# Performance work log

Measured on AMD Instinct MI355X. Metric: run time of the kernel, lower is better.

The kernel has to match this reference:

```python
import jax, jax.numpy as jnp
from jax import lax
import numpy as np

B, T, N, HORIZON = 64, 12, 512, 12
IN_DIM = 1; OUT_DIM = 1; YCOV = 1
RNN = 64; MEM_NUM = 20; MEM_DIM = 64; EMB = 10; CHEB_K = 3
DEC_DIM = RNN + MEM_DIM  # 128


def _xavier(key, shape):
    fan_in, fan_out = shape[0], shape[-1]
    std = float(np.sqrt(2.0 / (fan_in + fan_out)))
    return jax.random.normal(key, shape, dtype=jnp.float32) * std


def _cheb_feats(A, x, batched):
    mm = (lambda a, v: jnp.einsum('bnm,bmc->bnc', a, v)) if batched else (lambda a, v: jnp.einsum('nm,bmc->bnc', a, v))
    gs = [x, mm(A, x)]
    for _ in range(CHEB_K - 2):
        gs.append(2.0 * mm(A, gs[-1]) - gs[-2])
    return jnp.concatenate(gs, axis=-1)


def _agcn(x, A, W, b, batched):
    return _cheb_feats(A, x, batched) @ W + b


def _cell(x, state, A, Wg, bg, Wu, bu, batched):
    # AGCRN GRU cell
    hid = state.shape[-1]
    inp = jnp.concatenate([x, state], axis=-1)
    z_r = jax.nn.sigmoid(_agcn(inp, A, Wg, bg, batched))
    z, r = z_r[..., :hid], z_r[..., hid:]
    cand = jnp.concatenate([x, z * state], axis=-1)
    hc = jnp.tanh(_agcn(cand, A, Wu, bu, batched))
    return r * state + (1.0 - r) * hc


def _encode(x, A, Wg, bg, Wu, bu):
    # x: [B,T,N,C] -> last hidden state [B,N,RNN]
    xt = jnp.swapaxes(x, 0, 1)  # [T,B,N,C]
    init = jnp.zeros((x.shape[0], x.shape[2], RNN), x.dtype)
    def step(state, xt_):
        h = _cell(xt_, state, A, Wg, bg, Wu, bu, batched=False)
        return h, None
    h_t, _ = lax.scan(step, init, xt)
    return h_t


def _query_memory(h_t, Memory, Wq):
    q = h_t @ Wq                                   # [B,N,mem_dim]
    att = jax.nn.softmax(q @ Memory.T, axis=-1)    # [B,N,mem_num]
    value = att @ Memory                           # [B,N,mem_dim]
    _, ind = lax.top_k(att, 2)
    pos = Memory[ind[..., 0]]                      # [B,N,mem_dim]
    return value, pos


def setup_inputs() -> dict:
    key = jax.random.key(0)
    ks = jax.random.split(key, 20)
    x = jax.random.normal(ks[0], (B, T, N, IN_DIM), dtype=jnp.float32)
    x_cov = jax.random.normal(ks[1], (B, T, N, 1), dtype=jnp.float32)
    x_his = jax.random.normal(ks[2], (B, T, N, IN_DIM), dtype=jnp.float32)
    y_cov = jax.random.normal(ks[3], (B, HORIZON, N, YCOV), dtype=jnp.float32)
    a = jax.random.uniform(ks[4], (N, N), dtype=jnp.float32)
    adj = a / jnp.sum(a, axis=-1, keepdims=True)
    enc_in = IN_DIM + RNN
    dec_in = OUT_DIM + YCOV + DEC_DIM
    return {
        'x': x, 'x_cov': x_cov, 'x_his': x_his, 'y_cov': y_cov, 'adj': adj,
        'enc_gate_W': _xavier(ks[5], (CHEB_K * enc_in, 2 * RNN)),
        'enc_gate_b': jnp.zeros((2 * RNN,), jnp.float32),
        'enc_upd_W': _xavier(ks[6], (CHEB_K * enc_in, RNN)),
        'enc_upd_b': jnp.zeros((RNN,), jnp.float32),
        'dec_gate_W': _xavier(ks[7], (CHEB_K * dec_in, 2 * DEC_DIM)),
        'dec_gate_b': jnp.zeros((2 * DEC_DIM,), jnp.float32),
        'dec_upd_W': _xavier(ks[8], (CHEB_K * dec_in, DEC_DIM)),
        'dec_upd_b': jnp.zeros((DEC_DIM,), jnp.float32),
        'Memory': _xavier(ks[9], (MEM_NUM, MEM_DIM)),
        'Wq': _xavier(ks[10], (RNN, MEM_DIM)),
        'hyper_W': _xavier(ks[11], (DEC_DIM, EMB)),
        'hyper_b': jnp.zeros((EMB,), jnp.float32),
        'lat_W': _xavier(ks[12], (MEM_DIM, 1)),
        'lat_b': jnp.zeros((1,), jnp.float32),
        'proj_W': _xavier(ks[13], (DEC_DIM, OUT_DIM)),
        'proj_b': jnp.zeros((OUT_DIM,), jnp.float32),
    }


def reference(x, x_cov, x_his, y_cov, adj,
              enc_gate_W, enc_gate_b, enc_upd_W, enc_upd_b,
              dec_gate_W, dec_gate_b, dec_upd_W, dec_upd_b,
              Memory, Wq, hyper_W, hyper_b, lat_W, lat_b, proj_W, proj_b):
    # --- encoder on x and x_his (shared weights, single static support) ---
    h_t = _encode(x, adj, enc_gate_W, enc_gate_b, enc_upd_W, enc_upd_b)
    h_att, pos = _query_memory(h_t, Memory, Wq)
    h_his_t = _encode(x_his, adj, enc_gate_W, enc_gate_b, enc_upd_W, enc_upd_b)
    _, pos_his = _query_memory(h_his_t, Memory, Wq)
    # schema==1 latent distance head (sigmoid activation)
    latent_dis = jax.nn.sigmoid(((pos - pos_his) @ lat_W + lat_b)[..., 0])  # [B,N]
    # --- adaptive decoder support from hypernetwork ---
    h_aug = jnp.concatenate([h_t, h_att], axis=-1)          # [B,N,DEC_DIM]
    node_emb = h_aug @ hyper_W + hyper_b                    # [B,N,EMB]
    support = jax.nn.softmax(jax.nn.relu(jnp.einsum('bnc,bmc->bnm', node_emb, node_emb)), axis=-1)  # [B,N,N]
    # --- decoder rollout (inference path, no teacher forcing) ---
    go0 = jnp.zeros((x.shape[0], N, OUT_DIM), x.dtype)
    ycov_t = jnp.swapaxes(y_cov, 0, 1)  # [HORIZON,B,N,YCOV]
    def dec_step(carry, yc):
        go, h = carry
        xt = jnp.concatenate([go, yc], axis=-1)
        h = _cell(xt, h, support, dec_gate_W, dec_gate_b, dec_upd_W, dec_upd_b, batched=True)
        go = h @ proj_W + proj_b
        return (go, h), go
    _, outs = lax.scan(dec_step, (go0, h_aug), ycov_t)
    output = jnp.swapaxes(outs, 0, 1)  # [B,HORIZON,N,OUT_DIM]
    return output, latent_dis
```

## Files before the change

### kernel.cpp

```cpp
#include <hip/hip_runtime.h>
#include <hip/hip_bf16.h>


typedef __attribute__((ext_vector_type(8))) short s8v;
typedef __attribute__((ext_vector_type(4))) float f4v;
typedef __attribute__((ext_vector_type(4))) unsigned short u4v;

__device__ __forceinline__ float b2f(unsigned short u){
  union{unsigned int i; float f;} v; v.i = ((unsigned int)u)<<16; return v.f;
}
__device__ __forceinline__ unsigned short f2b(float f){
  union{float f; unsigned int i;} v; v.f = f;
  unsigned int r = v.i + 0x7fff + ((v.i >> 16) & 1);
  return (unsigned short)(r >> 16);
}

__global__ void k_zero16(uint4* p, int n){
  int i = blockIdx.x*256 + threadIdx.x;
  if (i < n) p[i] = make_uint4(0,0,0,0);
}


__global__ void k_reorderF(const float* __restrict__ W, float* __restrict__ Wr,
                           int HC, int NEX, int SEGW, int J){
  int idx = blockIdx.x*256 + threadIdx.x;
  int K = 3*SEGW;
  if (idx >= K*J) return;
  int k = idx / J, j = idx - k*J;
  int seg = k / SEGW, c = k - seg*SEGW;
  int CIN = HC + NEX;
  float v = 0.f;
  if (c < HC)       v = W[(size_t)(seg*CIN + NEX + c)*J + j];
  else if (c < CIN) v = W[(size_t)(seg*CIN + (c-HC))*J + j];
  Wr[(size_t)k*J + j] = v;
}

__global__ __launch_bounds__(256) void k_a2e(const float* __restrict__ A,
                                             float* __restrict__ A2e){
  __shared__ __align__(16) float As[32][132];
  __shared__ __align__(16) float Bs[32][132];
  int t = threadIdx.x;
  int r0 = (blockIdx.x & 3) * 128;
  int c0 = (blockIdx.x >> 2) * 128;
  int tr = t & 15, tc = t >> 4;
  float acc[8][8];
  #pragma unroll
  for (int i=0;i<8;i++)
    #pragma unroll
    for (int j=0;j<8;j++) acc[i][j]=0.f;
  for (int k0=0;k0<512;k0+=32){
    #pragma unroll
    for (int i=0;i<4;i++){
      int s = t + i*256;
      int r = s >> 3, kq = s & 7;
      float4 v = *(const float4*)(A + (size_t)(r0+r)*512 + k0 + kq*4);
      As[kq*4+0][r]=v.x; As[kq*4+1][r]=v.y; As[kq*4+2][r]=v.z; As[kq*4+3][r]=v.w;
    }
    #pragma unroll
    for (int i=0;i<4;i++){
      int s = t + i*256;
      int k = s >> 5, cq = s & 31;
      float4 v = *(const float4*)(A + (size_t)(k0+k)*512 + c0 + cq*4);
      *(float4*)&Bs[k][cq*4] = v;
    }
    __syncthreads();
    #pragma unroll 8
    for (int k=0;k<32;k++){
      float a[8], b[8];
      *(float4*)&a[0] = *(const float4*)&As[k][tr*4];
      *(float4*)&a[4] = *(const float4*)&As[k][64+tr*4];
      *(float4*)&b[0] = *(const float4*)&Bs[k][tc*4];
      *(float4*)&b[4] = *(const float4*)&Bs[k][64+tc*4];
      #pragma unroll
      for (int i=0;i<8;i++)
        #pragma unroll
        for (int j=0;j<8;j++) acc[i][j] += a[i]*b[j];
    }
    __syncthreads();
  }
  #pragma unroll
  for (int i=0;i<8;i++){
    int r = r0 + (i<4 ? tr*4+i : 64+tr*4+i-4);
    #pragma unroll
    for (int j=0;j<8;j++){
      int c = c0 + (j<4 ? tc*4+j : 64+tc*4+j-4);
      A2e[(size_t)r*512 + c] = 2.f*acc[i][j] - (r==c ? 1.f : 0.f);
    }
  }
}

__global__ __launch_bounds__(256,2) void k_mm2F(
    const float* __restrict__ A, const float* __restrict__ A2e,
    const float* __restrict__ hsrc,
    const float* __restrict__ xa, const float* __restrict__ xb,
    int tstep, float* __restrict__ feats)
{
  __shared__ __align__(16) float As[32][132];
  __shared__ __align__(16) float A2s[32][132];
  __shared__ __align__(16) float Bs[32][68];
  const int t = threadIdx.x;
  const int bb = blockIdx.z;
  const int n0 = blockIdx.x * 128;
  const int tr = t & 15, tc = t >> 4;
  const int xrow = t & 127, xmat = t >> 7;
  const float* xp = (bb < 64) ? (xa + ((size_t)bb*12 + tstep)*512)
                              : (xb + ((size_t)(bb-64)*12 + tstep)*512);
  float acc[2][2][4][4];
  #pragma unroll
  for (int m=0;m<2;m++)
    #pragma unroll
    for (int rg=0;rg<2;rg++)
      #pragma unroll
      for (int i=0;i<4;i++)
        #pragma unroll
        for (int j=0;j<4;j++) acc[m][rg][i][j]=0.f;
  float xacc = 0.f;

  for (int k0=0;k0<512;k0+=32){
    #pragma unroll
    for (int i=0;i<4;i++){
      int s = t + i*256;
      int r = s >> 3, kq = s & 7;
      float4 v = *(const float4*)(A + (size_t)(n0+r)*512 + k0 + kq*4);
      As[kq*4+0][r]=v.x; As[kq*4+1][r]=v.y; As[kq*4+2][r]=v.z; As[kq*4+3][r]=v.w;
      float4 w = *(const float4*)(A2e + (size_t)(n0+r)*512 + k0 + kq*4);
      A2s[kq*4+0][r]=w.x; A2s[kq*4+1][r]=w.y; A2s[kq*4+2][r]=w.z; A2s[kq*4+3][r]=w.w;
    }
    #pragma unroll
    for (int i=0;i<2;i++){
      int s = t + i*256;
      int k = s >> 4, cq = s & 15;
      float4 v = *(const float4*)(hsrc + (size_t)(bb*512 + k0 + k)*64 + cq*4);
      *(float4*)&Bs[k][cq*4] = v;
    }
    if (t < 32) Bs[t][64] = xp[k0 + t];
    __syncthreads();
    #pragma unroll 4
    for (int k=0;k<32;k++){
      float a1[8], a2[8], b[4];
      *(float4*)&a1[0] = *(const float4*)&As[k][tr*4];
      *(float4*)&a1[4] = *(const float4*)&As[k][64+tr*4];
      *(float4*)&a2[0] = *(const float4*)&A2s[k][tr*4];
      *(float4*)&a2[4] = *(const float4*)&A2s[k][64+tr*4];
      *(float4*)&b[0]  = *(const float4*)&Bs[k][tc*4];
      #pragma unroll
      for (int rg=0;rg<2;rg++)
        #pragma unroll
        for (int i=0;i<4;i++)
          #pragma unroll
          for (int j=0;j<4;j++){
            acc[0][rg][i][j] += a1[rg*4+i]*b[j];
            acc[1][rg][i][j] += a2[rg*4+i]*b[j];
          }
      xacc += (xmat ? A2s[k][xrow] : As[k][xrow]) * Bs[k][64];
    }
    if ((k0 >> 7) == (int)blockIdx.x){
      for (int s=t; s<544; s+=256){
        int k = s/17, q = s - k*17;
        float4 v;
        if (q < 16) v = *(const float4*)&Bs[k][q*4];
        else        v = make_float4(Bs[k][64], 0.f, 0.f, 0.f);
        *(float4*)(feats + (size_t)(bb*512 + k0 + k)*204 + q*4) = v;
      }
    }
    __syncthreads();
  }
  #pragma unroll
  for (int rg=0;rg<2;rg++){
    #pragma unroll
    for (int i=0;i<4;i++){
      int row = n0 + rg*64 + tr*4 + i;
      float* fr = feats + (size_t)(bb*512 + row)*204;
      float4 v;
      v.x=acc[0][rg][i][0]; v.y=acc[0][rg][i][1];
      v.z=acc[0][rg][i][2]; v.w=acc[0][rg][i][3];
      *(float4*)(fr + 68 + tc*4) = v;
      v.x=acc[1][rg][i][0]; v.y=acc[1][rg][i][1];
      v.z=acc[1][rg][i][2]; v.w=acc[1][rg][i][3];
      *(float4*)(fr + 136 + tc*4) = v;
    }
  }
  feats[(size_t)(bb*512 + n0 + xrow)*204 + (xmat ? 136 : 68) + 64] = xacc;
}

__global__ __launch_bounds__(256) void k_gwG(
    const float* __restrict__ feats, const float* __restrict__ Wr,
    const float* __restrict__ bias,
    const float* __restrict__ hbuf, float* __restrict__ zh, float* __restrict__ rbuf)
{
  __shared__ __align__(16) float As[17][132];
  __shared__ __align__(16) float Ws[17][132];
  const int t = threadIdx.x;
  const int row0 = blockIdx.x * 128;
  const int tr = t & 15, tc = t >> 4;
  float acc[2][2][4][4];
  #pragma unroll
  for (int rg=0;rg<2;rg++)
    #pragma unroll
    for (int cg=0;cg<2;cg++)
      #pragma unroll
      for (int i=0;i<4;i++)
        #pragma unroll
        for (int j=0;j<4;j++) acc[rg][cg][i][j]=0.f;
  for (int kc=0; kc<204; kc+=17){
    for (int s=t; s<2176; s+=256){
      int r = s/17, k = s - r*17;
      As[k][r] = feats[(size_t)(row0+r)*204 + kc + k];
    }
    for (int s=t; s<2176; s+=256){
      int k = s >> 7, j = s & 127;
      Ws[k][j] = Wr[(size_t)(kc+k)*128 + j];
    }
    __syncthreads();
    #pragma unroll
    for (int k=0;k<17;k++){
      float a[8], w[8];
      *(float4*)&a[0] = *(const float4*)&As[k][tr*4];
      *(float4*)&a[4] = *(const float4*)&As[k][64+tr*4];
      *(float4*)&w[0] = *(const float4*)&Ws[k][tc*4];
      *(float4*)&w[4] = *(const float4*)&Ws[k][64+tc*4];
      #pragma unroll
      for (int rg=0;rg<2;rg++)
        #pragma unroll
        for (int i=0;i<4;i++)
          #pragma unroll
          for (int cg=0;cg<2;cg++)
            #pragma unroll
            for (int j=0;j<4;j++)
              acc[rg][cg][i][j] += a[rg*4+i]*w[cg*4+j];
    }
    __syncthreads();
  }
  float bj0[4], bj1[4];
  #pragma unroll
  for (int j=0;j<4;j++){ bj0[j] = bias[tc*4+j]; bj1[j] = bias[64+tc*4+j]; }
  #pragma unroll
  for (int rg=0;rg<2;rg++){
    #pragma unroll
    for (int i=0;i<4;i++){
      int row = row0 + rg*64 + tr*4 + i;
      float4 h4 = *(const float4*)(hbuf + (size_t)row*64 + tc*4);
      float hv[4] = {h4.x,h4.y,h4.z,h4.w};
      float4 oz, orr;
      float z[4], rr[4];
      #pragma unroll
      for (int j=0;j<4;j++){
        z[j]  = 1.f/(1.f + __expf(-(acc[rg][0][i][j] + bj0[j])));
        rr[j] = 1.f/(1.f + __expf(-(acc[rg][1][i][j] + bj1[j])));
      }
      oz.x=z[0]*hv[0]; oz.y=z[1]*hv[1]; oz.z=z[2]*hv[2]; oz.w=z[3]*hv[3];
      orr.x=rr[0]; orr.y=rr[1]; orr.z=rr[2]; orr.w=rr[3];
      *(float4*)(zh   + (size_t)row*64 + tc*4) = oz;
      *(float4*)(rbuf + (size_t)row*64 + tc*4) = orr;
    }
  }
}

__global__ __launch_bounds__(256) void k_gwU(
    const float* __restrict__ feats, const float* __restrict__ Wr,
    const float* __restrict__ bias,
    float* __restrict__ henc, const float* __restrict__ rbuf)
{
  __shared__ __align__(16) float As[17][132];
  __shared__ __align__(16) float Ws[17][68];
  const int t = threadIdx.x;
  const int row0 = blockIdx.x * 128;
  const int tr = t & 15, tc = t >> 4;
  float acc[2][4][4];
  #pragma unroll
  for (int rg=0;rg<2;rg++)
    #pragma unroll
    for (int i=0;i<4;i++)
      #pragma unroll
      for (int j=0;j<4;j++) acc[rg][i][j]=0.f;
  for (int kc=0; kc<204; kc+=17){
    for (int s=t; s<2176; s+=256){
      int r = s/17, k = s - r*17;
      As[k][r] = feats[(size_t)(row0+r)*204 + kc + k];
    }
    for (int s=t; s<1088; s+=256){
      int k = s >> 6, j = s & 63;
      Ws[k][j] = Wr[(size_t)(kc+k)*64 + j];
    }
    __syncthreads();
    #pragma unroll
    for (int k=0;k<17;k++){
      float a[8], w[4];
      *(float4*)&a[0] = *(const float4*)&As[k][tr*4];
      *(float4*)&a[4] = *(const float4*)&As[k][64+tr*4];
      *(float4*)&w[0] = *(const float4*)&Ws[k][tc*4];
      #pragma unroll
      for (int rg=0;rg<2;rg++)
        #pragma unroll
        for (int i=0;i<4;i++)
          #pragma unroll
          for (int j=0;j<4;j++)
            acc[rg][i][j] += a[rg*4+i]*w[j];
    }
    __syncthreads();
  }
  float bj[4];
  #pragma unroll
  for (int j=0;j<4;j++) bj[j] = bias[tc*4+j];
  #pragma unroll
  for (int rg=0;rg<2;rg++){
    #pragma unroll
    for (int i=0;i<4;i++){
      int row = row0 + rg*64 + tr*4 + i;
      float4 h4 = *(const float4*)(henc + (size_t)row*64 + tc*4);
      float4 r4 = *(const float4*)(rbuf + (size_t)row*64 + tc*4);
      float hv[4] = {h4.x,h4.y,h4.z,h4.w};
      float rv[4] = {r4.x,r4.y,r4.z,r4.w};
      float ov[4];
      #pragma unroll
      for (int j=0;j<4;j++){
        float hc = 1.f - 2.f/(__expf(2.f*(acc[rg][i][j] + bj[j])) + 1.f);
        ov[j] = rv[j]*hv[j] + (1.f - rv[j])*hc;
      }
      float4 o; o.x=ov[0]; o.y=ov[1]; o.z=ov[2]; o.w=ov[3];
      *(float4*)(henc + (size_t)row*64 + tc*4) = o;
    }
  }
}


__global__ void k_reorderB(const float* __restrict__ W, unsigned short* __restrict__ Wr,
                           int HC, int NEX, int C, int KP, int J){
  int idx = blockIdx.x*256 + threadIdx.x;
  if (idx >= J*KP) return;
  int j = idx / KP, kp = idx - j*KP;
  float v = 0.f;
  if (kp < 3*C){
    int seg = kp / C, c = kp - seg*C;
    int CIN = HC + NEX;
    if (c < HC)       v = W[(size_t)(seg*CIN + NEX + c)*J + j];
    else if (c < CIN) v = W[(size_t)(seg*CIN + (c-HC))*J + j];
  }
  Wr[(size_t)j*KP + kp] = f2b(v);
}

template<int C16, bool BETA>
__global__ __launch_bounds__(256) void k_mmB(
    const unsigned short* __restrict__ M, long long mstride,
    unsigned short* fC, int C3, int xseg, int oseg,
    unsigned short* fR, int KP, float alpha)
{
  constexpr int C = C16*16;
  constexpr int BIT = (C*4 + 255)/256;
  __shared__ unsigned short Bs[C*40];
  const int t = threadIdx.x;
  const int w = t >> 6, L = t & 63, lm = L & 15, q = L >> 4;
  const int bb = blockIdx.z;
  const int n0 = blockIdx.x * 128;
  const unsigned short* Mb = M + (size_t)bb * mstride;
  unsigned short* fCb = fC + (size_t)bb * C3 * 512;
  const unsigned short* Xb = fCb + (size_t)xseg * C * 512;
  const unsigned short* Yb = fCb;
  unsigned short* Ob = fCb + (size_t)oseg * C * 512;
  const int rw = n0 + w*32;

  f4v acc[2][C16];
  #pragma unroll
  for (int i=0;i<2;i++)
    #pragma unroll
    for (int j=0;j<C16;j++)
      #pragma unroll
      for (int r=0;r<4;r++) acc[i][j][r] = 0.f;

  s8v breg[BIT];
  const size_t ar0 = (size_t)(rw + lm)*512 + q*8;
  const size_t ar1 = (size_t)(rw + 16 + lm)*512 + q*8;

  #pragma unroll
  for (int i=0;i<BIT;i++){
    int s = t + i*256;
    if (s < C*4) breg[i] = *(const s8v*)(Xb + (size_t)(s>>2)*512 + (s&3)*8);
  }
  s8v a0 = *(const s8v*)(Mb + ar0);
  s8v a1 = *(const s8v*)(Mb + ar1);

  for (int ks=0; ks<16; ks++){
    #pragma unroll
    for (int i=0;i<BIT;i++){
      int s = t + i*256;
      if (s < C*4) *(s8v*)&Bs[(s>>2)*40 + (s&3)*8] = breg[i];
    }
    __syncthreads();
    const int kn = (ks < 15) ? (ks+1)*32 : 0;
    #pragma unroll
    for (int i=0;i<BIT;i++){
      int s = t + i*256;
      if (s < C*4) breg[i] = *(const s8v*)(Xb + (size_t)(s>>2)*512 + kn + (s&3)*8);
    }
    s8v a0n = *(const s8v*)(Mb + ar0 + kn);
    s8v a1n = *(const s8v*)(Mb + ar1 + kn);
    #pragma unroll
    for (int ct=0; ct<C16; ct++){
      s8v b = *(const s8v*)&Bs[(ct*16+lm)*40 + q*8];
      acc[0][ct] = __builtin_amdgcn_mfma_f32_16x16x32_bf16(a0, b, acc[0][ct], 0,0,0);
      acc[1][ct] = __builtin_amdgcn_mfma_f32_16x16x32_bf16(a1, b, acc[1][ct], 0,0,0);
    }
    __syncthreads();
    a0 = a0n; a1 = a1n;
  }
  #pragma unroll
  for (int rt=0; rt<2; rt++){
    const int m0 = rw + rt*16 + q*4;
    #pragma unroll
    for (int ct=0; ct<C16; ct++){
      const int c = ct*16 + lm;
      u4v o;
      if (BETA){
        u4v y = *(const u4v*)(Yb + (size_t)c*512 + m0);
        #pragma unroll
        for (int r=0;r<4;r++) o[r] = f2b(alpha*acc[rt][ct][r] - b2f(y[r]));
      } else {
        #pragma unroll
        for (int r=0;r<4;r++) o[r] = f2b(acc[rt][ct][r]);
      }
      *(u4v*)(Ob + (size_t)c*512 + m0) = o;
      const size_t rbase = (size_t)(bb*512 + m0)*KP + oseg*C + c;
      #pragma unroll
      for (int r=0;r<4;r++) fR[rbase + (size_t)r*KP] = o[r];
    }
  }
}

template<int KSTEPS, int JT16, int MODE, int HC>
__global__ __launch_bounds__(256) void k_gwB(
    unsigned short* fR, int KP,
    const unsigned short* __restrict__ Wr, const float* __restrict__ bias,
    unsigned short* fC, int C3,
    float* hC, float* rbuf)
{
  constexpr int JT = JT16*16;
  constexpr int BIT = JT*4/256;
  __shared__ unsigned short Bs[JT*40];
  const int t = threadIdx.x;
  const int w = t >> 6, L = t & 63, lm = L & 15, q = L >> 4;
  const int row0 = blockIdx.x * 128;
  const int j0 = blockIdx.y * JT;
  const int rw = row0 + w*32;

  f4v acc[2][JT16];
  #pragma unroll
  for (int i=0;i<2;i++)
    #pragma unroll
    for (int j=0;j<JT16;j++)
      #pragma unroll
      for (int r=0;r<4;r++) acc[i][j][r] = 0.f;

  s8v breg[BIT];
  const unsigned short* Wb = Wr + (size_t)j0*KP;
  const size_t ar0 = (size_t)(rw + lm)*KP + q*8;
  const size_t ar1 = (size_t)(rw + 16 + lm)*KP + q*8;

  #pragma unroll
  for (int i=0;i<BIT;i++){
    int s = t + i*256;
    breg[i] = *(const s8v*)(Wb + (size_t)(s>>2)*KP + (s&3)*8);
  }
  s8v a0 = *(const s8v*)(fR + ar0);
  s8v a1 = *(const s8v*)(fR + ar1);

  for (int ks=0; ks<KSTEPS; ks++){
    #pragma unroll
    for (int i=0;i<BIT;i++){
      int s = t + i*256;
      *(s8v*)&Bs[(s>>2)*40 + (s&3)*8] = breg[i];
    }
    __syncthreads();
    const int kn = (ks < KSTEPS-1) ? (ks+1)*32 : 0;
    #pragma unroll
    for (int i=0;i<BIT;i++){
      int s = t + i*256;
      breg[i] = *(const s8v*)(Wb + (size_t)(s>>2)*KP + kn + (s&3)*8);
    }
    s8v a0n = *(const s8v*)(fR + ar0 + kn);
    s8v a1n = *(const s8v*)(fR + ar1 + kn);
    #pragma unroll
    for (int ct=0; ct<JT16; ct++){
      s8v b = *(const s8v*)&Bs[(ct*16+lm)*40 + q*8];
      acc[0][ct] = __builtin_amdgcn_mfma_f32_16x16x32_bf16(a0, b, acc[0][ct], 0,0,0);
      acc[1][ct] = __builtin_amdgcn_mfma_f32_16x16x32_bf16(a1, b, acc[1][ct], 0,0,0);
    }
    __syncthreads();
    a0 = a0n; a1 = a1n;
  }
  #pragma unroll
  for (int rt=0; rt<2; rt++){
    const int m0 = rw + rt*16 + q*4;
    const int bb = m0 >> 9, n = m0 & 511;
    #pragma unroll
    for (int ct=0; ct<JT16; ct++){
      const int j = j0 + ct*16 + lm;
      const float bj = bias[j];
      if (MODE == 0){
        if (j < HC){
          f4v h4 = *(const f4v*)(hC + ((size_t)bb*HC + j)*512 + n);
          u4v o;
          #pragma unroll
          for (int r=0;r<4;r++){
            float s = 1.f/(1.f + __expf(-(acc[rt][ct][r] + bj)));
            float zh = s * h4[r];
            o[r] = f2b(zh);
            fR[(size_t)(m0+r)*KP + j] = o[r];
          }
          *(u4v*)(fC + ((size_t)bb*C3 + j)*512 + n) = o;
        } else {
          f4v rv;
          #pragma unroll
          for (int r=0;r<4;r++) rv[r] = 1.f/(1.f + __expf(-(acc[rt][ct][r] + bj)));
          *(f4v*)(rbuf + ((size_t)bb*HC + (j-HC))*512 + n) = rv;
        }
      } else {
        f4v h4 = *(const f4v*)(hC + ((size_t)bb*HC + j)*512 + n);
        f4v r4 = *(const f4v*)(rbuf + ((size_t)bb*HC + j)*512 + n);
        u4v o; f4v hn;
        #pragma unroll
        for (int r=0;r<4;r++){
          float e = __expf(2.f*(acc[rt][ct][r] + bj));
          float hc_ = 1.f - 2.f/(e + 1.f);
          hn[r] = r4[r]*h4[r] + (1.f - r4[r])*hc_;
          o[r] = f2b(hn[r]);
          fR[(size_t)(m0+r)*KP + j] = o[r];
        }
        *(f4v*)(hC + ((size_t)bb*HC + j)*512 + n) = hn;
        *(u4v*)(fC + ((size_t)bb*C3 + j)*512 + n) = o;
      }
    }
  }
}


__global__ void k_extras_dec(const float* __restrict__ yc,
    unsigned short* fR, unsigned short* fC, int tstep){
  int rr = blockIdx.x*256 + threadIdx.x;
  int bb = rr >> 9, n = rr & 511;
  unsigned short u = f2b(yc[((size_t)bb*12 + tstep)*512 + n]);
  fR[(size_t)rr*448 + 129] = u;
  fC[((size_t)bb*432 + 129)*512 + n] = u;
}
__global__ void k_fix_go(unsigned short* fR, unsigned short* fC){
  int rr = blockIdx.x*256 + threadIdx.x;
  int bb = rr >> 9, n = rr & 511;
  fR[(size_t)rr*448 + 128] = 0;
  fC[((size_t)bb*432 + 128)*512 + n] = 0;
}

__global__ __launch_bounds__(256) void k_query(const float* __restrict__ hR,
      const float* __restrict__ Wq, const float* __restrict__ Mem,
      float* __restrict__ hCd, unsigned short* fR, unsigned short* fC,
      int* __restrict__ it, int* __restrict__ ih){
  int sub = threadIdx.x >> 6, lane = threadIdx.x & 63;
  int row = blockIdx.x*4 + sub;
  __shared__ float sh[4][64], sq[4][64], ss[4][20];
  float hv = hR[(size_t)row*64 + lane];
  sh[sub][lane] = hv;
  __syncthreads();
  float qv = 0.f;
  for (int c=0;c<64;c++) qv += sh[sub][c]*Wq[c*64 + lane];
  sq[sub][lane] = qv;
  __syncthreads();
  if (lane < 20){
    float s = 0.f;
    for (int j=0;j<64;j++) s += sq[sub][j]*Mem[lane*64 + j];
    ss[sub][lane] = s;
  }
  __syncthreads();
  float mx = -1e30f; int am = 0;
  for (int m=0;m<20;m++){ float s = ss[sub][m]; if (s > mx){ mx = s; am = m; } }
  float sum = 0.f;
  for (int m=0;m<20;m++) sum += __expf(ss[sub][m]-mx);
  float inv = 1.f/sum;
  float v = 0.f;
  for (int m=0;m<20;m++) v += __expf(ss[sub][m]-mx)*inv*Mem[m*64 + lane];
  int bb = row >> 9, n = row & 511;
  if (bb < 64){
    hCd[((size_t)bb*128 + lane)*512 + n] = hv;
    hCd[((size_t)bb*128 + 64 + lane)*512 + n] = v;
    fR[(size_t)row*448 + lane] = f2b(hv);
    fR[(size_t)row*448 + 64 + lane] = f2b(v);
    fC[((size_t)bb*432 + lane)*512 + n] = f2b(hv);
    fC[((size_t)bb*432 + 64 + lane)*512 + n] = f2b(v);
    if (lane==0) it[row] = am;
  } else {
    if (lane==0) ih[row - 32768] = am;
  }
}

__global__ void k_latent(const int* __restrict__ it, const int* __restrict__ ih,
                         const float* __restrict__ Mem,
                         const float* __restrict__ lW, const float* __restrict__ lb,
                         float* __restrict__ outl){
  int row = blockIdx.x*256 + threadIdx.x;
  int i1 = it[row], i2 = ih[row];
  float a = lb[0];
  for (int c=0;c<64;c++) a += (Mem[i1*64+c]-Mem[i2*64+c])*lW[c];
  outl[row] = 1.f/(1.f + __expf(-a));
}

__global__ __launch_bounds__(256) void k_emb(const float* __restrict__ hCd,
    const float* __restrict__ hW, const float* __restrict__ hb, float* __restrict__ emb){
  __shared__ float sW[1280];
  int t = threadIdx.x;
  for (int s=t; s<1280; s+=256) sW[s] = hW[s];
  __syncthreads();
  int rr = blockIdx.x*256 + t;
  int bb = rr >> 9, n = rr & 511;
  float a[10];
  #pragma unroll
  for (int e=0;e<10;e++) a[e] = hb[e];
  for (int c=0;c<128;c++){
    float v = hCd[((size_t)bb*128 + c)*512 + n];
    #pragma unroll
    for (int e=0;e<10;e++) a[e] += v*sW[c*10+e];
  }
  #pragma unroll
  for (int e=0;e<10;e++) emb[(size_t)rr*10 + e] = a[e];
}

__global__ __launch_bounds__(256) void k_support(const float* __restrict__ emb,
                                                 unsigned short* __restrict__ sup){
  int b = blockIdx.x >> 9;
  int n = blockIdx.x & 511;
  int t = threadIdx.x;
  __shared__ float se[5120];
  __shared__ float red[8];
  for (int s = t; s < 5120; s += 256) se[s] = emb[(size_t)b*5120 + s];
  __syncthreads();
  float en[10];
  #pragma unroll
  for (int i=0;i<10;i++) en[i] = se[n*10+i];
  float s0=0.f, s1=0.f;
  #pragma unroll
  for (int i=0;i<10;i++){ s0 += en[i]*se[t*10+i]; s1 += en[i]*se[(t+256)*10+i]; }
  s0 = fmaxf(s0, 0.f); s1 = fmaxf(s1, 0.f);
  float mx = fmaxf(s0, s1);
  for (int o=32;o>0;o>>=1) mx = fmaxf(mx, __shfl_down(mx, o));
  if ((t&63)==0) red[t>>6] = mx;
  __syncthreads();
  mx = fmaxf(fmaxf(red[0],red[1]), fmaxf(red[2],red[3]));
  float e0 = __expf(s0-mx), e1 = __expf(s1-mx);
  float sm = e0 + e1;
  for (int o=32;o>0;o>>=1) sm += __shfl_down(sm, o);
  if ((t&63)==0) red[4+(t>>6)] = sm;
  __syncthreads();
  sm = red[4]+red[5]+red[6]+red[7];
  float inv = 1.f/sm;
  size_t base = ((size_t)b*512 + n)*512;
  sup[base + t]       = f2b(e0*inv);
  sup[base + t + 256] = f2b(e1*inv);
}

__global__ __launch_bounds__(256) void k_proj(const float* __restrict__ hCd,
    const float* __restrict__ pW, const float* __restrict__ pb,
    unsigned short* fR, unsigned short* fC, float* __restrict__ out, int tstep){
  __shared__ float sW[128];
  int t = threadIdx.x;
  if (t < 128) sW[t] = pW[t];
  __syncthreads();
  int rr = blockIdx.x*256 + t;
  int bb = rr >> 9, n = rr & 511;
  float a = pb[0];
  for (int c=0;c<128;c++) a += hCd[((size_t)bb*128 + c)*512 + n]*sW[c];
  out[((size_t)bb*12 + tstep)*512 + n] = a;
  unsigned short u = f2b(a);
  fR[(size_t)rr*448 + 128] = u;
  fC[((size_t)bb*432 + 128)*512 + n] = u;
}

extern "C" void kernel_launch(void* const* d_in, const int* in_sizes, int n_in,
                              void* d_out, int out_size, void* d_ws, size_t ws_size,
                              hipStream_t stream) {
  const float* x     = (const float*)d_in[0];
  const float* x_his = (const float*)d_in[2];
  const float* y_cov = (const float*)d_in[3];
  const float* adj   = (const float*)d_in[4];
  const float* egW   = (const float*)d_in[5];
  const float* egb   = (const float*)d_in[6];
  const float* euW   = (const float*)d_in[7];
  const float* eub   = (const float*)d_in[8];
  const float* dgW   = (const float*)d_in[9];
  const float* dgb   = (const float*)d_in[10];
  const float* duW   = (const float*)d_in[11];
  const float* dub   = (const float*)d_in[12];
  const float* Mem   = (const float*)d_in[13];
  const float* Wq    = (const float*)d_in[14];
  const float* hW    = (const float*)d_in[15];
  const float* hb    = (const float*)d_in[16];
  const float* lW    = (const float*)d_in[17];
  const float* lb    = (const float*)d_in[18];
  const float* pW    = (const float*)d_in[19];
  const float* pb    = (const float*)d_in[20];
  float* out  = (float*)d_out;
  float* outl = out + 393216;

  char* base = (char*)d_ws;
  size_t off = 0;
  auto alloc = [&](size_t bytes)->char*{
    char* p = base + off; off = (off + bytes + 255) & ~(size_t)255; return p;
  };
  float* featsF = (float*)alloc(53477376);
  unsigned short* sup = (unsigned short*)featsF;
  float* emb = featsF + 8650752;
  int*   it  = (int*)(featsF + 9961472);
  int*   ih  = it + 32768;
  float* henc = (float*)alloc(16777216);
  float* zhF  = (float*)alloc(16777216);
  float* hCd  = zhF;
  float* rbF  = (float*)alloc(16777216);
  unsigned short* fR = (unsigned short*)alloc(29360128);
  unsigned short* fC = (unsigned short*)alloc(28311552);
  float* a2e = (float*)alloc(1048576);
  float* wr_egF = (float*)alloc(104448);
  float* wr_euF = (float*)alloc(52224);
  unsigned short* wr_dg = (unsigned short*)alloc(229376);
  unsigned short* wr_du = (unsigned short*)alloc(114688);
  if (ws_size < off) return;

  k_zero16<<<4096,256,0,stream>>>((uint4*)henc, 1048576);
  k_zero16<<<7168,256,0,stream>>>((uint4*)fR, 1835008);
  k_zero16<<<6912,256,0,stream>>>((uint4*)fC, 1769472);
  k_a2e<<<16,256,0,stream>>>(adj, a2e);
  k_reorderF<<<102,256,0,stream>>>(egW, wr_egF, 64,1,68,128);
  k_reorderF<<< 51,256,0,stream>>>(euW, wr_euF, 64,1,68,64);
  k_reorderB<<<448,256,0,stream>>>(dgW, wr_dg, 128,2,144,448,256);
  k_reorderB<<<224,256,0,stream>>>(duW, wr_du, 128,2,144,448,128);

  for (int t = 0; t < 12; t++){
    k_mm2F<<<dim3(4,1,128),256,0,stream>>>(adj, a2e, henc, x, x_his, t, featsF);
    k_gwG<<<512,256,0,stream>>>(featsF, wr_egF, egb, henc, zhF, rbF);
    k_mm2F<<<dim3(4,1,128),256,0,stream>>>(adj, a2e, zhF, x, x_his, t, featsF);
    k_gwU<<<512,256,0,stream>>>(featsF, wr_euF, eub, henc, rbF);
  }

  k_query<<<16384,256,0,stream>>>(henc, Wq, Mem, hCd, fR, fC, it, ih);
  k_latent<<<128,256,0,stream>>>(it, ih, Mem, lW, lb, outl);
  k_emb<<<128,256,0,stream>>>(hCd, hW, hb, emb);
  k_support<<<32768,256,0,stream>>>(emb, sup);
  k_fix_go<<<128,256,0,stream>>>(fR, fC);

  for (int t = 0; t < 12; t++){
    k_extras_dec<<<128,256,0,stream>>>(y_cov, fR, fC, t);
    k_mmB<9,false><<<dim3(4,1,64),256,0,stream>>>(sup, 262144, fC, 432, 0, 1, fR, 448, 1.f);
    k_mmB<9,true ><<<dim3(4,1,64),256,0,stream>>>(sup, 262144, fC, 432, 1, 2, fR, 448, 2.f);
    k_gwB<14,16,0,128><<<dim3(256,1),256,0,stream>>>(fR, 448, wr_dg, dgb, fC, 432, hCd, rbF);
    k_mmB<9,false><<<dim3(4,1,64),256,0,stream>>>(sup, 262144, fC, 432, 0, 1, fR, 448, 1.f);
    k_mmB<9,true ><<<dim3(4,1,64),256,0,stream>>>(sup, 262144, fC, 432, 1, 2, fR, 448, 2.f);
    k_gwB<14,8,1,128><<<dim3(256,1),256,0,stream>>>(fR, 448, wr_du, dub, fC, 432, hCd, rbF);
    k_proj<<<128,256,0,stream>>>(hCd, pW, pb, fR, fC, out, t);
  }
}
```

Before: 7.285 ms.

## Process two batch sequences per block in encoder Chebyshev matmul

Each k_mm2F block now computes the graph products for two batch entries (the x and x_his streams, z and z+64), so every A and A2e tile staged in LDS is used twice and the grid halves. Accumulator registers double, and the launch-bounds occupancy hint is dropped with unroll lowered to 2. The A tile loads become strided scalar loads that write float4 into LDS without transposed scatter stores, in both k_a2e and k_mm2F. This trades uncoalesced global reads and higher register pressure for less global traffic on the adjacency matrices.

```diff
diff --git a/kernel.cpp b/kernel.cpp
--- a/kernel.cpp
+++ b/kernel.cpp
@@ -52,9 +52,11 @@
     #pragma unroll
     for (int i=0;i<4;i++){
       int s = t + i*256;
-      int r = s >> 3, kq = s & 7;
-      float4 v = *(const float4*)(A + (size_t)(r0+r)*512 + k0 + kq*4);
-      As[kq*4+0][r]=v.x; As[kq*4+1][r]=v.y; As[kq*4+2][r]=v.z; As[kq*4+3][r]=v.w;
+      int k = s & 31, rq = s >> 5;
+      const float* ap = A + (size_t)(r0 + rq*4)*512 + k0 + k;
+      float4 v;
+      v.x = ap[0]; v.y = ap[512]; v.z = ap[1024]; v.w = ap[1536];
+      *(float4*)&As[k][rq*4] = v;
     }
     #pragma unroll
     for (int i=0;i<4;i++){
@@ -89,7 +91,7 @@
   }
 }
 
-__global__ __launch_bounds__(256,2) void k_mm2F(
+__global__ __launch_bounds__(256) void k_mm2F(
     const float* __restrict__ A, const float* __restrict__ A2e,
     const float* __restrict__ hsrc,
     const float* __restrict__ xa, const float* __restrict__ xb,
@@ -97,90 +99,111 @@
 {
   __shared__ __align__(16) float As[32][132];
   __shared__ __align__(16) float A2s[32][132];
-  __shared__ __align__(16) float Bs[32][68];
+  __shared__ __align__(16) float Bs0[32][68];
+  __shared__ __align__(16) float Bs1[32][68];
   const int t = threadIdx.x;
-  const int bb = blockIdx.z;
+  const int z = blockIdx.z;
   const int n0 = blockIdx.x * 128;
   const int tr = t & 15, tc = t >> 4;
   const int xrow = t & 127, xmat = t >> 7;
-  const float* xp = (bb < 64) ? (xa + ((size_t)bb*12 + tstep)*512)
-                              : (xb + ((size_t)(bb-64)*12 + tstep)*512);
-  float acc[2][2][4][4];
+  const float* xp0 = xa + ((size_t)z*12 + tstep)*512;
+  const float* xp1 = xb + ((size_t)z*12 + tstep)*512;
+  float acc[2][2][2][4][4];
   #pragma unroll
   for (int m=0;m<2;m++)
     #pragma unroll
-    for (int rg=0;rg<2;rg++)
-      #pragma unroll
-      for (int i=0;i<4;i++)
-        #pragma unroll
-        for (int j=0;j<4;j++) acc[m][rg][i][j]=0.f;
-  float xacc = 0.f;
+    for (int b=0;b<2;b++)
+      #pragma unroll
+      for (int rg=0;rg<2;rg++)
+        #pragma unroll
+        for (int i=0;i<4;i++)
+          #pragma unroll
+          for (int j=0;j<4;j++) acc[m][b][rg][i][j]=0.f;
+  float xacc0 = 0.f, xacc1 = 0.f;
 
   for (int k0=0;k0<512;k0+=32){
     #pragma unroll
     for (int i=0;i<4;i++){
       int s = t + i*256;
-      int r = s >> 3, kq = s & 7;
-      float4 v = *(const float4*)(A + (size_t)(n0+r)*512 + k0 + kq*4);
-      As[kq*4+0][r]=v.x; As[kq*4+1][r]=v.y; As[kq*4+2][r]=v.z; As[kq*4+3][r]=v.w;
-      float4 w = *(const float4*)(A2e + (size_t)(n0+r)*512 + k0 + kq*4);
-      A2s[kq*4+0][r]=w.x; A2s[kq*4+1][r]=w.y; A2s[kq*4+2][r]=w.z; A2s[kq*4+3][r]=w.w;
+      int k = s & 31, rq = s >> 5;
+      const float* ap  = A   + (size_t)(n0 + rq*4)*512 + k0 + k;
+      const float* a2p = A2e + (size_t)(n0 + rq*4)*512 + k0 + k;
+      float4 v, w;
+      v.x = ap[0];  v.y = ap[512];  v.z = ap[1024];  v.w = ap[1536];
+      w.x = a2p[0]; w.y = a2p[512]; w.z = a2p[1024]; w.w = a2p[1536];
+      *(float4*)&As[k][rq*4]  = v;
+      *(float4*)&A2s[k][rq*4] = w;
     }
     #pragma unroll
     for (int i=0;i<2;i++){
       int s = t + i*256;
       int k = s >> 4, cq = s & 15;
-      float4 v = *(const float4*)(hsrc + (size_t)(bb*512 + k0 + k)*64 + cq*4);
-      *(float4*)&Bs[k][cq*4] = v;
-    }
-    if (t < 32) Bs[t][64] = xp[k0 + t];
-    __syncthreads();
-    #pragma unroll 4
+      *(float4*)&Bs0[k][cq*4] = *(const float4*)(hsrc + (size_t)(z*512 + k0 + k)*64 + cq*4);
+      *(float4*)&Bs1[k][cq*4] = *(const float4*)(hsrc + (size_t)((z+64)*512 + k0 + k)*64 + cq*4);
+    }
+    if (t < 32)      Bs0[t][64]    = xp0[k0 + t];
+    else if (t < 64) Bs1[t-32][64] = xp1[k0 + t - 32];
+    __syncthreads();
+    #pragma unroll 2
     for (int k=0;k<32;k++){
-      float a1[8], a2[8], b[4];
+      float a1[8], a2[8], b0[4], b1[4];
       *(float4*)&a1[0] = *(const float4*)&As[k][tr*4];
       *(float4*)&a1[4] = *(const float4*)&As[k][64+tr*4];
       *(float4*)&a2[0] = *(const float4*)&A2s[k][tr*4];
       *(float4*)&a2[4] = *(const float4*)&A2s[k][64+tr*4];
-      *(float4*)&b[0]  = *(const float4*)&Bs[k][tc*4];
+      *(float4*)&b0[0] = *(const float4*)&Bs0[k][tc*4];
+      *(float4*)&b1[0] = *(const float4*)&Bs1[k][tc*4];
       #pragma unroll
       for (int rg=0;rg<2;rg++)
         #pragma unroll
         for (int i=0;i<4;i++)
           #pragma unroll
           for (int j=0;j<4;j++){
-            acc[0][rg][i][j] += a1[rg*4+i]*b[j];
-            acc[1][rg][i][j] += a2[rg*4+i]*b[j];
+            acc[0][0][rg][i][j] += a1[rg*4+i]*b0[j];
+            acc[0][1][rg][i][j] += a1[rg*4+i]*b1[j];
+            acc[1][0][rg][i][j] += a2[rg*4+i]*b0[j];
+            acc[1][1][rg][i][j] += a2[rg*4+i]*b1[j];
           }
-      xacc += (xmat ? A2s[k][xrow] : As[k][xrow]) * Bs[k][64];
+      float am = xmat ? A2s[k][xrow] : As[k][xrow];
+      xacc0 += am * Bs0[k][64];
+      xacc1 += am * Bs1[k][64];
     }
     if ((k0 >> 7) == (int)blockIdx.x){
-      for (int s=t; s<544; s+=256){
-        int k = s/17, q = s - k*17;
+      for (int s=t; s<1088; s+=256){
+        int sb = (s >= 544) ? 1 : 0;
+        int ss = s - sb*544;
+        int kk = ss/17, q = ss - kk*17;
+        int bb = z + sb*64;
         float4 v;
-        if (q < 16) v = *(const float4*)&Bs[k][q*4];
-        else        v = make_float4(Bs[k][64], 0.f, 0.f, 0.f);
-        *(float4*)(feats + (size_t)(bb*512 + k0 + k)*204 + q*4) = v;
+        if (q < 16) v = sb ? *(const float4*)&Bs1[kk][q*4] : *(const float4*)&Bs0[kk][q*4];
+        else        v = make_float4(sb ? Bs1[kk][64] : Bs0[kk][64], 0.f, 0.f, 0.f);
+        *(float4*)(feats + (size_t)(bb*512 + k0 + kk)*204 + q*4) = v;
       }
     }
     __syncthreads();
   }
   #pragma unroll
-  for (int rg=0;rg<2;rg++){
-    #pragma unroll
-    for (int i=0;i<4;i++){
-      int row = n0 + rg*64 + tr*4 + i;
-      float* fr = feats + (size_t)(bb*512 + row)*204;
-      float4 v;
-      v.x=acc[0][rg][i][0]; v.y=acc[0][rg][i][1];
-      v.z=acc[0][rg][i][2]; v.w=acc[0][rg][i][3];
-      *(float4*)(fr + 68 + tc*4) = v;
-      v.x=acc[1][rg][i][0]; v.y=acc[1][rg][i][1];
-      v.z=acc[1][rg][i][2]; v.w=acc[1][rg][i][3];
-      *(float4*)(fr + 136 + tc*4) = v;
-    }
-  }
-  feats[(size_t)(bb*512 + n0 + xrow)*204 + (xmat ? 136 : 68) + 64] = xacc;
+  for (int bbi=0;bbi<2;bbi++){
+    const int bb = z + bbi*64;
+    #pragma unroll
+    for (int rg=0;rg<2;rg++){
+      #pragma unroll
+      for (int i=0;i<4;i++){
+        int row = n0 + rg*64 + tr*4 + i;
+        float* fr = feats + (size_t)(bb*512 + row)*204;
+        float4 v;
+        v.x=acc[0][bbi][rg][i][0]; v.y=acc[0][bbi][rg][i][1];
+        v.z=acc[0][bbi][rg][i][2]; v.w=acc[0][bbi][rg][i][3];
+        *(float4*)(fr + 68 + tc*4) = v;
+        v.x=acc[1][bbi][rg][i][0]; v.y=acc[1][bbi][rg][i][1];
+        v.z=acc[1][bbi][rg][i][2]; v.w=acc[1][bbi][rg][i][3];
+        *(float4*)(fr + 136 + tc*4) = v;
+      }
+    }
+  }
+  const int xoff = (xmat ? 136 : 68) + 64;
+  feats[(size_t)(z*512 + n0 + xrow)*204 + xoff]        = xacc0;
+  feats[(size_t)((z+64)*512 + n0 + xrow)*204 + xoff]   = xacc1;
 }
 
 __global__ __launch_bounds__(256) void k_gwG(
@@ -729,9 +752,9 @@
   k_reorderB<<<224,256,0,stream>>>(duW, wr_du, 128,2,144,448,128);
 
   for (int t = 0; t < 12; t++){
-    k_mm2F<<<dim3(4,1,128),256,0,stream>>>(adj, a2e, henc, x, x_his, t, featsF);
+    k_mm2F<<<dim3(4,1,64),256,0,stream>>>(adj, a2e, henc, x, x_his, t, featsF);
     k_gwG<<<512,256,0,stream>>>(featsF, wr_egF, egb, henc, zhF, rbF);
-    k_mm2F<<<dim3(4,1,128),256,0,stream>>>(adj, a2e, zhF, x, x_his, t, featsF);
+    k_mm2F<<<dim3(4,1,64),256,0,stream>>>(adj, a2e, zhF, x, x_his, t, featsF);
     k_gwU<<<512,256,0,stream>>>(featsF, wr_euF, eub, henc, rbF);
   }
 
```

New measurement: 7.289 ms. Within noise of the previous version (+0.1%).
